# Kernel optimization log

Measured on AMD Instinct MI355X. Metric: run time of the kernel, lower is better.

## Reference

```python
import jax, jax.numpy as jnp
import numpy as np

N = 100000      # nodes
E = 1600000     # edges
NF, EF = 8, 4   # raw node/edge feature dims
HID = 64        # hidden_dim
HEADS = 4
C = HID // HEADS  # per-head channels = 16
L = 3           # num_layers
NEG_SLOPE = 0.2 # PyG GATConv leaky_relu slope
LN_EPS = 1e-5


def setup_inputs():
    key = jax.random.key(0)
    ks = jax.random.split(key, 16)
    s = 0.1
    return {
        "x": jax.random.normal(ks[0], (N, NF), dtype=jnp.float32),
        "edge_index": jax.random.randint(ks[1], (2, E), 0, N, dtype=jnp.int32),
        "edge_attr": jax.random.normal(ks[2], (E, EF), dtype=jnp.float32),
        "node_w": jax.random.normal(ks[3], (NF, HID), dtype=jnp.float32) * s,
        "node_b": jnp.zeros((HID,), jnp.float32),
        "edge_w": jax.random.normal(ks[4], (EF, HID), dtype=jnp.float32) * s,
        "edge_b": jnp.zeros((HID,), jnp.float32),
        "lin_w": jax.random.normal(ks[5], (L, HID, HEADS * C), dtype=jnp.float32) * s,
        "lin_edge_w": jax.random.normal(ks[6], (L, HID, HEADS * C), dtype=jnp.float32) * s,
        "att_src": jax.random.normal(ks[7], (L, HEADS, C), dtype=jnp.float32) * s,
        "att_dst": jax.random.normal(ks[8], (L, HEADS, C), dtype=jnp.float32) * s,
        "att_edge": jax.random.normal(ks[9], (L, HEADS, C), dtype=jnp.float32) * s,
        "gat_bias": jnp.zeros((L, HID), jnp.float32),
        "ln_gamma": jnp.ones((L, HID), jnp.float32),
        "ln_beta": jnp.zeros((L, HID), jnp.float32),
    }


def _layer_norm(x, g, b):
    mu = jnp.mean(x, axis=-1, keepdims=True)
    var = jnp.mean(jnp.square(x - mu), axis=-1, keepdims=True)
    return (x - mu) * jax.lax.rsqrt(var + LN_EPS) * g + b


def _gat_conv(x, src, dst, e_proj, lin_w, lin_edge_w, a_src_w, a_dst_w, a_edge_w, bias):
    """PyG GATConv (concat=True, edge_dim, self-loops with fill='mean').
    x: [N,HID]; src/dst: [E'] (already include self loops); e_proj: [E',HID]."""
    n = x.shape[0]
    xs = (x @ lin_w).reshape(n, HEADS, C)                    # [N,H,C]
    ea = (e_proj @ lin_edge_w).reshape(-1, HEADS, C)         # [E',H,C]
    a_src = jnp.einsum('nhc,hc->nh', xs, a_src_w)            # [N,H]
    a_dst = jnp.einsum('nhc,hc->nh', xs, a_dst_w)            # [N,H]
    a_edge = jnp.einsum('ehc,hc->eh', ea, a_edge_w)          # [E',H]
    alpha = a_src[src] + a_dst[dst] + a_edge                 # [E',H]
    alpha = jax.nn.leaky_relu(alpha, NEG_SLOPE)
    # segment softmax over edges sharing a destination node
    amax = jax.ops.segment_max(alpha, dst, num_segments=n)   # [N,H]
    ex = jnp.exp(alpha - amax[dst])
    denom = jax.ops.segment_sum(ex, dst, num_segments=n)     # [N,H]
    w = ex / (denom[dst] + 1e-16)                            # [E',H]
    msg = xs[src] * w[:, :, None]                            # [E',H,C]
    out = jax.ops.segment_sum(msg, dst, num_segments=n)      # [N,H,C]
    return out.reshape(n, HEADS * C) + bias


def reference(x, edge_index, edge_attr, node_w, node_b, edge_w, edge_b,
              lin_w, lin_edge_w, att_src, att_dst, att_edge, gat_bias,
              ln_gamma, ln_beta):
    h = x @ node_w + node_b                                  # [N,HID]
    e = edge_attr @ edge_w + edge_b                          # [E,HID]
    src, dst = edge_index[0], edge_index[1]
    # add self loops once (same for all layers); edge_attr fill = per-dst mean
    ones = jnp.ones((E,), h.dtype)
    deg = jax.ops.segment_sum(ones, dst, num_segments=N)     # [N]
    e_mean = jax.ops.segment_sum(e, dst, num_segments=N) / jnp.maximum(deg, 1.0)[:, None]
    loop = jnp.arange(N, dtype=src.dtype)
    src_f = jnp.concatenate([src, loop])
    dst_f = jnp.concatenate([dst, loop])
    e_f = jnp.concatenate([e, e_mean], axis=0)               # [E+N,HID]
    for i in range(L):
        residual = h
        h = _gat_conv(h, src_f, dst_f, e_f, lin_w[i], lin_edge_w[i],
                      att_src[i], att_dst[i], att_edge[i], gat_bias[i])
        h = _layer_norm(h + residual, ln_gamma[i], ln_beta[i])
        h = jax.nn.relu(h)
    return h
```

## Files before the change

kernel.cpp:

```cpp
#include <hip/hip_runtime.h>


#define LRELU_SLOPE 0.2f
#define LOG2E 1.4426950408889634f
#define P1B 512
#define NBKT_MAX 512

typedef float f32x2 __attribute__((ext_vector_type(2)));

#ifdef __has_builtin
#if __has_builtin(__builtin_amdgcn_fdot2_f32_bf16)
#define HAS_BF16DOT 1
#endif
#endif
#ifndef HAS_BF16DOT
#define HAS_BF16DOT 0
#endif

#if HAS_BF16DOT
typedef __bf16 bf16x2_t __attribute__((ext_vector_type(2)));
#endif

__device__ __forceinline__ f32x2 fp8lo(unsigned int v) {
    return __builtin_amdgcn_cvt_pk_f32_fp8((int)v, false);
}
__device__ __forceinline__ f32x2 fp8hi(unsigned int v) {
    return __builtin_amdgcn_cvt_pk_f32_fp8((int)v, true);
}
__device__ __forceinline__ ushort f2bf(float x) {
    unsigned int b = __float_as_uint(x);
    return (ushort)((b + 0x7fffu + ((b >> 16) & 1u)) >> 16);
}
__device__ __forceinline__ unsigned int pack2bf(float a, float b) {
    return (unsigned int)f2bf(a) | ((unsigned int)f2bf(b) << 16);
}
__device__ __forceinline__ float bf_lo(unsigned int v) { return __uint_as_float(v << 16); }
__device__ __forceinline__ float bf_hi(unsigned int v) { return __uint_as_float(v & 0xffff0000u); }

__device__ __forceinline__ float dot2bf(unsigned int a, unsigned int b, float c) {
#if HAS_BF16DOT
    return __builtin_amdgcn_fdot2_f32_bf16(__builtin_bit_cast(bf16x2_t, a),
                                           __builtin_bit_cast(bf16x2_t, b), c, false);
#else
    return fmaf(bf_lo(a), bf_lo(b), fmaf(bf_hi(a), bf_hi(b), c));
#endif
}

__global__ void k_smallw(const float* __restrict__ lin_edge_w,
                         const float* __restrict__ att_edge,
                         const float* __restrict__ edge_w,
                         const float* __restrict__ edge_b,
                         float* __restrict__ Mc)
{
    __shared__ float we[3][64][4];
    int t = threadIdx.x;
    if (t < 192) {
        int l = t >> 6, k = t & 63;
        for (int h = 0; h < 4; ++h) {
            float acc = 0.f;
            #pragma unroll
            for (int c = 0; c < 16; ++c)
                acc = fmaf(lin_edge_w[l*4096 + k*64 + h*16 + c],
                           att_edge[l*64 + h*16 + c], acc);
            we[l][k][h] = acc;
        }
    }
    __syncthreads();
    if (t < 48) {
        int l = t >> 4, k4 = (t >> 2) & 3, h = t & 3;
        float acc = 0.f;
        for (int k = 0; k < 64; ++k)
            acc = fmaf(edge_w[k4*64 + k], we[l][k][h], acc);
        Mc[l*16 + k4*4 + h] = acc * LOG2E;
    }
    if (t >= 64 && t < 76) {
        int u = t - 64, l = u >> 2, h = u & 3;
        float acc = 0.f;
        for (int k = 0; k < 64; ++k)
            acc = fmaf(edge_b[k], we[l][k][h], acc);
        Mc[48 + l*4 + h] = acc * LOG2E;
    }
}

__global__ void k_node_proj(const float* __restrict__ x, const float* __restrict__ nw,
                            const float* __restrict__ nb, ushort* __restrict__ hbf,
                            int n_nodes)
{
    int idx = blockIdx.x * blockDim.x + threadIdx.x;
    int n = idx >> 6, j = idx & 63;
    if (n >= n_nodes) return;
    float acc = nb[j];
    #pragma unroll
    for (int k = 0; k < 8; ++k) acc = fmaf(x[n*8 + k], nw[k*64 + j], acc);
    hbf[(size_t)n*64 + j] = f2bf(acc);
}

__global__ __launch_bounds__(256) void k_hist1(const int* __restrict__ dst,
                                               int* __restrict__ C,
                                               int E, int chunk, int nbkt) {
    __shared__ int h[NBKT_MAX];
    int b = blockIdx.x, t = threadIdx.x;
    for (int i = t; i < nbkt; i += 256) h[i] = 0;
    __syncthreads();
    int e0 = b*chunk, e1 = min(e0 + chunk, E);
    for (int e = e0 + t; e < e1; e += 256)
        atomicAdd(&h[dst[e] >> 8], 1);
    __syncthreads();
    for (int i = t; i < nbkt; i += 256) C[i*P1B + b] = h[i];
}

__global__ void k_scanA(const int* __restrict__ in, int* __restrict__ out,
                        int* __restrict__ bsum, int n) {
    __shared__ int s[1024];
    int i = blockIdx.x*1024 + threadIdx.x;
    s[threadIdx.x] = (i < n) ? in[i] : 0;
    __syncthreads();
    for (int off = 1; off < 1024; off <<= 1) {
        int t = (threadIdx.x >= off) ? s[threadIdx.x - off] : 0;
        __syncthreads();
        s[threadIdx.x] += t;
        __syncthreads();
    }
    if (i < n) out[i] = s[threadIdx.x];
    if (threadIdx.x == 1023) bsum[blockIdx.x] = s[1023];
}

__global__ void k_scanB(int* bsum, int nb) {
    __shared__ int s[1024];
    int t = threadIdx.x;
    int own = (t < nb) ? bsum[t] : 0;
    s[t] = own;
    __syncthreads();
    for (int off = 1; off < 1024; off <<= 1) {
        int v = (t >= off) ? s[t - off] : 0;
        __syncthreads();
        s[t] += v;
        __syncthreads();
    }
    if (t < nb) bsum[t] = s[t] - own;
}

__global__ void k_scanC(int* __restrict__ S, const int* __restrict__ bsum, int n) {
    int i = blockIdx.x*1024 + threadIdx.x;
    if (i < n) S[i] += bsum[blockIdx.x];
}

__global__ __launch_bounds__(256) void k_scat1(const int* __restrict__ dst,
        const int* __restrict__ srcv, const float4* __restrict__ ea,
        const int* __restrict__ S, uint2* __restrict__ brec,
        int E, int chunk, int nbkt) {
    __shared__ int base[NBKT_MAX];
    __shared__ int cur[NBKT_MAX];
    int b = blockIdx.x, t = threadIdx.x;
    for (int i = t; i < nbkt; i += 256) {
        int flat = i*P1B + b;
        base[i] = flat ? S[flat - 1] : 0;
        cur[i] = 0;
    }
    __syncthreads();
    int e0 = b*chunk, e1 = min(e0 + chunk, E);
    for (int e = e0 + t; e < e1; e += 256) {
        int d = dst[e];
        int bin = d >> 8;
        int lr = atomicAdd(&cur[bin], 1);
        int slot = base[bin] + lr;
        float4 v = ea[e];
        unsigned int p = (unsigned int)__builtin_amdgcn_cvt_pk_fp8_f32(v.x, v.y, 0, false);
        p = (unsigned int)__builtin_amdgcn_cvt_pk_fp8_f32(v.z, v.w, (int)p, true);
        uint2 r;
        r.x = (unsigned int)srcv[e] | ((unsigned int)(d & 255) << 24);
        r.y = p;
        brec[slot] = r;
    }
}

__global__ __launch_bounds__(256) void k_csr(const uint2* __restrict__ brec,
        const int* __restrict__ S, uint2* __restrict__ recs,
        int* __restrict__ rowptr, int nbkt, int NN, int E) {
    int bkt = blockIdx.x, t = threadIdx.x;
    __shared__ int cnt[256], exc[256], cur[256], ssc[256];
    int seg_b = bkt ? S[bkt*P1B - 1] : 0;
    int seg_e = S[(bkt + 1)*P1B - 1];
    cnt[t] = 0; cur[t] = 0;
    __syncthreads();
    for (int i = seg_b + t; i < seg_e; i += 256)
        atomicAdd(&cnt[brec[i].x >> 24], 1);
    __syncthreads();
    ssc[t] = cnt[t];
    __syncthreads();
    for (int off = 1; off < 256; off <<= 1) {
        int v = (t >= off) ? ssc[t - off] : 0;
        __syncthreads();
        ssc[t] += v;
        __syncthreads();
    }
    exc[t] = ssc[t] - cnt[t];
    __syncthreads();
    int g = bkt*256 + t;
    if (g < NN) rowptr[g] = seg_b + exc[t];
    if (bkt == nbkt - 1 && t == 0) rowptr[NN] = E;
    for (int i = seg_b + t; i < seg_e; i += 256) {
        uint2 r = brec[i];
        int dl = (int)(r.x >> 24);
        int slot = seg_b + exc[dl] + atomicAdd(&cur[dl], 1);
        r.x &= 0x00FFFFFFu;
        recs[slot] = r;
    }
}

__global__ void k_eamean(const int* __restrict__ rowptr, const uint2* __restrict__ recs,
                         float4* __restrict__ ea_mean, int n) {
    int i = blockIdx.x*blockDim.x + threadIdx.x;
    if (i >= n) return;
    int b = rowptr[i], e = rowptr[i + 1];
    float sx = 0.f, sy = 0.f, sz = 0.f, sw = 0.f;
    for (int s = b; s < e; ++s) {
        unsigned int p = recs[s].y;
        f32x2 lo = fp8lo(p), hi = fp8hi(p);
        sx += lo.x; sy += lo.y; sz += hi.x; sw += hi.y;
    }
    float inv = (e > b) ? 1.f / (float)(e - b) : 0.f;
    ea_mean[i] = make_float4(sx*inv, sy*inv, sz*inv, sw*inv);
}

__global__ __launch_bounds__(256) void k_proj(const ushort* __restrict__ hbf,
        const float* __restrict__ lw,
        const float* __restrict__ asw,
        const float* __restrict__ adw,
        ushort* __restrict__ xs2, float* __restrict__ a_src4,
        float* __restrict__ a_dst4, int n_nodes)
{
    __shared__ unsigned int Wp[2048];
    for (int i = threadIdx.x; i < 2048; i += 256) {
        int k2 = i >> 6, c = i & 63;
        Wp[i] = pack2bf(lw[(k2*2)*64 + c], lw[(k2*2+1)*64 + c]);
    }
    __syncthreads();
    int lane = threadIdx.x & 63, wid = threadIdx.x >> 6;
    float as_w = asw[lane] * LOG2E, ad_w = adw[lane] * LOG2E;
    int nquads = (n_nodes + 3) >> 2;
    int nlast = n_nodes - 1;
    for (int q = blockIdx.x*4 + wid; q < nquads; q += gridDim.x*4) {
        int n0 = q << 2;
        int n1 = min(n0+1, nlast), n2 = min(n0+2, nlast), n3 = min(n0+3, nlast);
        const uint4* r0p = (const uint4*)(hbf + (size_t)n0*64);
        const uint4* r1p = (const uint4*)(hbf + (size_t)n1*64);
        const uint4* r2p = (const uint4*)(hbf + (size_t)n2*64);
        const uint4* r3p = (const uint4*)(hbf + (size_t)n3*64);
        float acc0 = 0.f, acc1 = 0.f, acc2 = 0.f, acc3 = 0.f;
        #pragma unroll
        for (int qq = 0; qq < 8; ++qq) {
            uint4 u0 = r0p[qq], u1 = r1p[qq], u2 = r2p[qq], u3 = r3p[qq];
            unsigned int w0 = Wp[(qq*4+0)*64 + lane];
            unsigned int w1 = Wp[(qq*4+1)*64 + lane];
            unsigned int w2 = Wp[(qq*4+2)*64 + lane];
            unsigned int w3 = Wp[(qq*4+3)*64 + lane];
            acc0 = dot2bf(u0.w, w3, dot2bf(u0.z, w2, dot2bf(u0.y, w1, dot2bf(u0.x, w0, acc0))));
            acc1 = dot2bf(u1.w, w3, dot2bf(u1.z, w2, dot2bf(u1.y, w1, dot2bf(u1.x, w0, acc1))));
            acc2 = dot2bf(u2.w, w3, dot2bf(u2.z, w2, dot2bf(u2.y, w1, dot2bf(u2.x, w0, acc2))));
            acc3 = dot2bf(u3.w, w3, dot2bf(u3.z, w2, dot2bf(u3.y, w1, dot2bf(u3.x, w0, acc3))));
        }
        xs2[(size_t)n0*64 + lane] = f2bf(acc0);
        xs2[(size_t)n1*64 + lane] = f2bf(acc1);
        xs2[(size_t)n2*64 + lane] = f2bf(acc2);
        xs2[(size_t)n3*64 + lane] = f2bf(acc3);
        #define ARED(ACC, NJ) { \
            float ps = (ACC)*as_w, pd = (ACC)*ad_w; \
            ps += __shfl_xor(ps,1,16); pd += __shfl_xor(pd,1,16); \
            ps += __shfl_xor(ps,2,16); pd += __shfl_xor(pd,2,16); \
            ps += __shfl_xor(ps,4,16); pd += __shfl_xor(pd,4,16); \
            ps += __shfl_xor(ps,8,16); pd += __shfl_xor(pd,8,16); \
            if ((lane & 15) == 0) { \
                a_src4[(NJ)*4 + (lane>>4)] = ps; \
                a_dst4[(NJ)*4 + (lane>>4)] = pd; \
            } }
        ARED(acc0, n0) ARED(acc1, n1) ARED(acc2, n2) ARED(acc3, n3)
        #undef ARED
    }
}

__global__ __launch_bounds__(256) void k_gat(const uint4* __restrict__ xs4,
        const float* __restrict__ a_src4, const float* __restrict__ a_dst4,
        const int* __restrict__ rowptr, const uint2* __restrict__ recs,
        const float4* __restrict__ ea_mean,
        const float* __restrict__ Mc,
        const float* __restrict__ c0,
        const float* __restrict__ bias, const float* __restrict__ lng,
        const float* __restrict__ lnb,
        const ushort* __restrict__ hbf_in, ushort* __restrict__ hbf_out,
        float* __restrict__ out_f32, int last, int n_nodes)
{
    int n = blockIdx.x*4 + (threadIdx.x >> 6);
    if (n >= n_nodes) return;
    int lane = threadIdx.x & 63;
    int k8  = lane & 7;
    int hB  = k8 >> 1;
    int grp = lane >> 3;
    int cb = k8 * 8;
    uint4 rr = *(const uint4*)(hbf_in + (size_t)n*64 + cb);
    float4 eam = ea_mean[n];
    float m0 = Mc[hB], m1 = Mc[4+hB], m2 = Mc[8+hB], m3 = Mc[12+hB];
    float c0v = c0[hB];
    float adv = a_dst4[n*4 + hB];
    float cc = c0v + adv;
    int rb = rowptr[n], re = rowptr[n + 1];

    float denL = 0.f;
    float a0=0.f,a1=0.f,a2=0.f,a3=0.f,a4=0.f,a5=0.f,a6=0.f,a7=0.f;

    if (rb < re) {
        int last_e = re - 1;
        int i0 = rb + grp;     i0 = (i0 > last_e) ? last_e : i0;
        uint2 rc = recs[i0];
        int i1 = rb + 8 + grp; i1 = (i1 > last_e) ? last_e : i1;
        uint2 rn = recs[i1];
        float asc = a_src4[(int)rc.x*4 + hB];
        uint4 xc = xs4[(unsigned)rc.x*8u + (unsigned)k8];
        #pragma unroll 2
        for (int b = rb; b < re; b += 8) {
            int i2 = b + 16 + grp; i2 = (i2 > last_e) ? last_e : i2;
            uint2 r2 = recs[i2];
            float asn = a_src4[(int)rn.x*4 + hB];
            uint4 xn = xs4[(unsigned)rn.x*8u + (unsigned)k8];
            f32x2 e01 = fp8lo(rc.y), e23 = fp8hi(rc.y);
            float al = fmaf(e01.x, m0, fmaf(e01.y, m1,
                       fmaf(e23.x, m2, fmaf(e23.y, m3, cc)))) + asc;
            al = fmaxf(al, LRELU_SLOPE * al);
            float ev = (b + grp < re) ? exp2f(al) : 0.f;
            denL += ev;
            a0 = fmaf(bf_lo(xc.x), ev, a0); a1 = fmaf(bf_hi(xc.x), ev, a1);
            a2 = fmaf(bf_lo(xc.y), ev, a2); a3 = fmaf(bf_hi(xc.y), ev, a3);
            a4 = fmaf(bf_lo(xc.z), ev, a4); a5 = fmaf(bf_hi(xc.z), ev, a5);
            a6 = fmaf(bf_lo(xc.w), ev, a6); a7 = fmaf(bf_hi(xc.w), ev, a7);
            rc = rn; rn = r2; asc = asn; xc = xn;
        }
    }
    denL += __shfl_xor(denL, 8); denL += __shfl_xor(denL, 16); denL += __shfl_xor(denL, 32);
    #define XR(A) A += __shfl_xor(A, 8); A += __shfl_xor(A, 16); A += __shfl_xor(A, 32);
    XR(a0) XR(a1) XR(a2) XR(a3) XR(a4) XR(a5) XR(a6) XR(a7)
    #undef XR
    float ael = (re > rb)
        ? fmaf(eam.x, m0, fmaf(eam.y, m1, fmaf(eam.z, m2, fmaf(eam.w, m3, c0v))))
        : 0.f;
    float alS = a_src4[n*4 + hB] + adv + ael;
    alS = fmaxf(alS, LRELU_SLOPE * alS);
    float evS = exp2f(alS);
    float denF = denL + evS;
    uint4 vs = xs4[(unsigned)n*8u + (unsigned)k8];
    a0 = fmaf(bf_lo(vs.x), evS, a0); a1 = fmaf(bf_hi(vs.x), evS, a1);
    a2 = fmaf(bf_lo(vs.y), evS, a2); a3 = fmaf(bf_hi(vs.y), evS, a3);
    a4 = fmaf(bf_lo(vs.z), evS, a4); a5 = fmaf(bf_hi(vs.z), evS, a5);
    a6 = fmaf(bf_lo(vs.w), evS, a6); a7 = fmaf(bf_hi(vs.w), evS, a7);
    float inv = 1.f / (denF + 1e-16f);
    const float4* bp = (const float4*)(bias + cb);
    float4 b0 = bp[0], b1 = bp[1];
    float o0 = a0*inv + b0.x + bf_lo(rr.x), o1 = a1*inv + b0.y + bf_hi(rr.x);
    float o2 = a2*inv + b0.z + bf_lo(rr.y), o3 = a3*inv + b0.w + bf_hi(rr.y);
    float o4 = a4*inv + b1.x + bf_lo(rr.z), o5 = a5*inv + b1.y + bf_hi(rr.z);
    float o6 = a6*inv + b1.z + bf_lo(rr.w), o7 = a7*inv + b1.w + bf_hi(rr.w);
    float s1 = o0+o1+o2+o3+o4+o5+o6+o7;
    s1 += __shfl_xor(s1, 1); s1 += __shfl_xor(s1, 2); s1 += __shfl_xor(s1, 4);
    float mu = s1 * 0.015625f;
    float d0=o0-mu,d1=o1-mu,d2=o2-mu,d3=o3-mu,d4=o4-mu,d5=o5-mu,d6=o6-mu,d7=o7-mu;
    float s2 = d0*d0+d1*d1+d2*d2+d3*d3+d4*d4+d5*d5+d6*d6+d7*d7;
    s2 += __shfl_xor(s2, 1); s2 += __shfl_xor(s2, 2); s2 += __shfl_xor(s2, 4);
    float rs = rsqrtf(s2 * 0.015625f + 1e-5f);
    const float4* gp = (const float4*)(lng + cb);
    const float4* zp = (const float4*)(lnb + cb);
    float4 g0 = gp[0], g1 = gp[1], z0 = zp[0], z1 = zp[1];
    float y0 = fmaxf(d0*rs*g0.x + z0.x, 0.f), y1 = fmaxf(d1*rs*g0.y + z0.y, 0.f);
    float y2 = fmaxf(d2*rs*g0.z + z0.z, 0.f), y3 = fmaxf(d3*rs*g0.w + z0.w, 0.f);
    float y4 = fmaxf(d4*rs*g1.x + z1.x, 0.f), y5 = fmaxf(d5*rs*g1.y + z1.y, 0.f);
    float y6 = fmaxf(d6*rs*g1.z + z1.z, 0.f), y7 = fmaxf(d7*rs*g1.w + z1.w, 0.f);
    if (lane < 8) {
        if (last) {
            float4* outp = (float4*)(out_f32 + (size_t)n*64 + cb);
            outp[0] = make_float4(y0, y1, y2, y3);
            outp[1] = make_float4(y4, y5, y6, y7);
        } else {
            uint4 pk;
            pk.x = pack2bf(y0, y1); pk.y = pack2bf(y2, y3);
            pk.z = pack2bf(y4, y5); pk.w = pack2bf(y6, y7);
            *(uint4*)(hbf_out + (size_t)n*64 + cb) = pk;
        }
    }
}

extern "C" void kernel_launch(void* const* d_in, const int* in_sizes, int n_in,
                              void* d_out, int out_size, void* d_ws, size_t ws_size,
                              hipStream_t stream) {
    const float* x          = (const float*)d_in[0];
    const int*   ei         = (const int*)d_in[1];
    const float* edge_attr  = (const float*)d_in[2];
    const float* node_w     = (const float*)d_in[3];
    const float* node_b     = (const float*)d_in[4];
    const float* edge_w     = (const float*)d_in[5];
    const float* edge_b     = (const float*)d_in[6];
    const float* lin_w      = (const float*)d_in[7];
    const float* lin_edge_w = (const float*)d_in[8];
    const float* att_src    = (const float*)d_in[9];
    const float* att_dst    = (const float*)d_in[10];
    const float* att_edge   = (const float*)d_in[11];
    const float* gat_bias   = (const float*)d_in[12];
    const float* ln_g       = (const float*)d_in[13];
    const float* ln_b       = (const float*)d_in[14];

    int NN = in_sizes[0] / 8;
    int E  = in_sizes[1] / 2;
    const int* src = ei;
    const int* dst = ei + E;

    int nbkt = (NN + 255) >> 8;
    int ntot = nbkt * P1B;
    int chunk = (E + P1B - 1) / P1B;

    char* wsp = (char*)d_ws;
    size_t off = 0;
    auto alloc = [&](size_t bytes) -> void* {
        off = (off + 255) & ~(size_t)255;
        void* p = wsp + off;
        off += bytes;
        return p;
    };
    ushort* h_bf    = (ushort*)alloc((size_t)NN * 64 * 2);
    ushort* xs2     = (ushort*)alloc((size_t)NN * 64 * 2);
    float*  a_src4  = (float*)alloc((size_t)NN * 4 * 4);
    float*  a_dst4  = (float*)alloc((size_t)NN * 4 * 4);
    uint2*  recs    = (uint2*)alloc((size_t)E * 8);
    uint2*  brec    = (uint2*)alloc((size_t)E * 8);
    float4* ea_mean = (float4*)alloc((size_t)NN * 16);
    int*    rowptr  = (int*)alloc((size_t)(NN + 1) * 4);
    int*    S       = (int*)alloc((size_t)ntot * 4);
    int*    bsum    = (int*)alloc(4096);
    float*  Mc      = (float*)alloc(256);

    k_smallw<<<1, 256, 0, stream>>>(lin_edge_w, att_edge, edge_w, edge_b, Mc);
    k_node_proj<<<(NN*64 + 255) / 256, 256, 0, stream>>>(x, node_w, node_b, h_bf, NN);
    k_hist1<<<P1B, 256, 0, stream>>>(dst, S, E, chunk, nbkt);
    int nsb = (ntot + 1023) / 1024;
    k_scanA<<<nsb, 1024, 0, stream>>>(S, S, bsum, ntot);
    k_scanB<<<1, 1024, 0, stream>>>(bsum, nsb);
    k_scanC<<<nsb, 1024, 0, stream>>>(S, bsum, ntot);
    k_scat1<<<P1B, 256, 0, stream>>>(dst, src, (const float4*)edge_attr,
                                     S, brec, E, chunk, nbkt);
    k_csr<<<nbkt, 256, 0, stream>>>(brec, S, recs, rowptr, nbkt, NN, E);
    k_eamean<<<(NN + 255) / 256, 256, 0, stream>>>(rowptr, recs, ea_mean, NN);

    for (int l = 0; l < 3; ++l) {
        k_proj<<<2048, 256, 0, stream>>>(h_bf, lin_w + l*4096, att_src + l*64,
                                         att_dst + l*64, xs2, a_src4, a_dst4, NN);
        k_gat<<<(NN + 3) / 4, 256, 0, stream>>>((const uint4*)xs2, a_src4, a_dst4,
                                                rowptr, recs, ea_mean,
                                                Mc + l*16, Mc + 48 + l*4,
                                                gat_bias + l*64, ln_g + l*64, ln_b + l*64,
                                                h_bf, h_bf, (float*)d_out,
                                                (l == 2) ? 1 : 0, NN);
    }
}
```

Baseline: 376.1 us.

## Fuse edge-attr mean into CSR build, register-cache proj weights, pack GAT FMAs

Measured after the change: 398.6 us. +6.0%, slower.

```diff
diff --git a/kernel.cpp b/kernel.cpp
--- a/kernel.cpp
+++ b/kernel.cpp
@@ -176,12 +176,15 @@
 
 __global__ __launch_bounds__(256) void k_csr(const uint2* __restrict__ brec,
         const int* __restrict__ S, uint2* __restrict__ recs,
-        int* __restrict__ rowptr, int nbkt, int NN, int E) {
+        int* __restrict__ rowptr, float4* __restrict__ ea_mean,
+        int nbkt, int NN, int E) {
     int bkt = blockIdx.x, t = threadIdx.x;
     __shared__ int cnt[256], exc[256], cur[256], ssc[256];
+    __shared__ float ea0[256], ea1[256], ea2[256], ea3[256];
     int seg_b = bkt ? S[bkt*P1B - 1] : 0;
     int seg_e = S[(bkt + 1)*P1B - 1];
     cnt[t] = 0; cur[t] = 0;
+    ea0[t] = 0.f; ea1[t] = 0.f; ea2[t] = 0.f; ea3[t] = 0.f;
     __syncthreads();
     for (int i = seg_b + t; i < seg_e; i += 256)
         atomicAdd(&cnt[brec[i].x >> 24], 1);
@@ -205,22 +208,16 @@
         int slot = seg_b + exc[dl] + atomicAdd(&cur[dl], 1);
         r.x &= 0x00FFFFFFu;
         recs[slot] = r;
-    }
-}
-
-__global__ void k_eamean(const int* __restrict__ rowptr, const uint2* __restrict__ recs,
-                         float4* __restrict__ ea_mean, int n) {
-    int i = blockIdx.x*blockDim.x + threadIdx.x;
-    if (i >= n) return;
-    int b = rowptr[i], e = rowptr[i + 1];
-    float sx = 0.f, sy = 0.f, sz = 0.f, sw = 0.f;
-    for (int s = b; s < e; ++s) {
-        unsigned int p = recs[s].y;
-        f32x2 lo = fp8lo(p), hi = fp8hi(p);
-        sx += lo.x; sy += lo.y; sz += hi.x; sw += hi.y;
-    }
-    float inv = (e > b) ? 1.f / (float)(e - b) : 0.f;
-    ea_mean[i] = make_float4(sx*inv, sy*inv, sz*inv, sw*inv);
+        f32x2 lo = fp8lo(r.y), hi = fp8hi(r.y);
+        atomicAdd(&ea0[dl], lo.x); atomicAdd(&ea1[dl], lo.y);
+        atomicAdd(&ea2[dl], hi.x); atomicAdd(&ea3[dl], hi.y);
+    }
+    __syncthreads();
+    if (g < NN) {
+        int dg = cnt[t];
+        float inv = dg ? 1.f / (float)dg : 0.f;
+        ea_mean[g] = make_float4(ea0[t]*inv, ea1[t]*inv, ea2[t]*inv, ea3[t]*inv);
+    }
 }
 
 __global__ __launch_bounds__(256) void k_proj(const ushort* __restrict__ hbf,
@@ -230,13 +227,11 @@
         ushort* __restrict__ xs2, float* __restrict__ a_src4,
         float* __restrict__ a_dst4, int n_nodes)
 {
-    __shared__ unsigned int Wp[2048];
-    for (int i = threadIdx.x; i < 2048; i += 256) {
-        int k2 = i >> 6, c = i & 63;
-        Wp[i] = pack2bf(lw[(k2*2)*64 + c], lw[(k2*2+1)*64 + c]);
-    }
-    __syncthreads();
     int lane = threadIdx.x & 63, wid = threadIdx.x >> 6;
+    unsigned int W[32];
+    #pragma unroll
+    for (int k2 = 0; k2 < 32; ++k2)
+        W[k2] = pack2bf(lw[(k2*2)*64 + lane], lw[(k2*2+1)*64 + lane]);
     float as_w = asw[lane] * LOG2E, ad_w = adw[lane] * LOG2E;
     int nquads = (n_nodes + 3) >> 2;
     int nlast = n_nodes - 1;
@@ -251,10 +246,8 @@
         #pragma unroll
         for (int qq = 0; qq < 8; ++qq) {
             uint4 u0 = r0p[qq], u1 = r1p[qq], u2 = r2p[qq], u3 = r3p[qq];
-            unsigned int w0 = Wp[(qq*4+0)*64 + lane];
-            unsigned int w1 = Wp[(qq*4+1)*64 + lane];
-            unsigned int w2 = Wp[(qq*4+2)*64 + lane];
-            unsigned int w3 = Wp[(qq*4+3)*64 + lane];
+            unsigned int w0 = W[qq*4+0], w1 = W[qq*4+1];
+            unsigned int w2 = W[qq*4+2], w3 = W[qq*4+3];
             acc0 = dot2bf(u0.w, w3, dot2bf(u0.z, w2, dot2bf(u0.y, w1, dot2bf(u0.x, w0, acc0))));
             acc1 = dot2bf(u1.w, w3, dot2bf(u1.z, w2, dot2bf(u1.y, w1, dot2bf(u1.x, w0, acc1))));
             acc2 = dot2bf(u2.w, w3, dot2bf(u2.z, w2, dot2bf(u2.y, w1, dot2bf(u2.x, w0, acc2))));
@@ -306,7 +299,7 @@
     int rb = rowptr[n], re = rowptr[n + 1];
 
     float denL = 0.f;
-    float a0=0.f,a1=0.f,a2=0.f,a3=0.f,a4=0.f,a5=0.f,a6=0.f,a7=0.f;
+    f32x2 a01 = {0.f, 0.f}, a23 = {0.f, 0.f}, a45 = {0.f, 0.f}, a67 = {0.f, 0.f};
 
     if (rb < re) {
         int last_e = re - 1;
@@ -328,13 +321,21 @@
             al = fmaxf(al, LRELU_SLOPE * al);
             float ev = (b + grp < re) ? exp2f(al) : 0.f;
             denL += ev;
-            a0 = fmaf(bf_lo(xc.x), ev, a0); a1 = fmaf(bf_hi(xc.x), ev, a1);
-            a2 = fmaf(bf_lo(xc.y), ev, a2); a3 = fmaf(bf_hi(xc.y), ev, a3);
-            a4 = fmaf(bf_lo(xc.z), ev, a4); a5 = fmaf(bf_hi(xc.z), ev, a5);
-            a6 = fmaf(bf_lo(xc.w), ev, a6); a7 = fmaf(bf_hi(xc.w), ev, a7);
+            f32x2 ev2; ev2.x = ev; ev2.y = ev;
+            f32x2 x01, x23, x45, x67;
+            x01.x = bf_lo(xc.x); x01.y = bf_hi(xc.x);
+            x23.x = bf_lo(xc.y); x23.y = bf_hi(xc.y);
+            x45.x = bf_lo(xc.z); x45.y = bf_hi(xc.z);
+            x67.x = bf_lo(xc.w); x67.y = bf_hi(xc.w);
+            a01 += x01 * ev2;
+            a23 += x23 * ev2;
+            a45 += x45 * ev2;
+            a67 += x67 * ev2;
             rc = rn; rn = r2; asc = asn; xc = xn;
         }
     }
+    float a0 = a01.x, a1 = a01.y, a2 = a23.x, a3 = a23.y;
+    float a4 = a45.x, a5 = a45.y, a6 = a67.x, a7 = a67.y;
     denL += __shfl_xor(denL, 8); denL += __shfl_xor(denL, 16); denL += __shfl_xor(denL, 32);
     #define XR(A) A += __shfl_xor(A, 8); A += __shfl_xor(A, 16); A += __shfl_xor(A, 32);
     XR(a0) XR(a1) XR(a2) XR(a3) XR(a4) XR(a5) XR(a6) XR(a7)
@@ -443,8 +444,7 @@
     k_scanC<<<nsb, 1024, 0, stream>>>(S, bsum, ntot);
     k_scat1<<<P1B, 256, 0, stream>>>(dst, src, (const float4*)edge_attr,
                                      S, brec, E, chunk, nbkt);
-    k_csr<<<nbkt, 256, 0, stream>>>(brec, S, recs, rowptr, nbkt, NN, E);
-    k_eamean<<<(NN + 255) / 256, 256, 0, stream>>>(rowptr, recs, ea_mean, NN);
+    k_csr<<<nbkt, 256, 0, stream>>>(brec, S, recs, rowptr, ea_mean, nbkt, NN, E);
 
     for (int l = 0; l < 3; ++l) {
         k_proj<<<2048, 256, 0, stream>>>(h_bf, lin_w + l*4096, att_src + l*64,
```
